# Optimization experiments

Measured on AMD Instinct MI355X. Metric: run time of the kernel, lower is better.

The kernel has to match this reference:

```python
import jax, jax.numpy as jnp
import numpy as np

EPS = 1e-5


def _cbr(z, W, bn, relu=True):
    # z: [b, Cin, L]; W: [Cout, Cin]; bn: [4, Cout] = (gamma, beta, mean, var)
    # 1x1 Conv2d (bias=False) over a [b, Cin, L, 1] tensor == channel matmul.
    y = jnp.einsum('oi,bil->bol', W, z)
    g, b_, m, v = bn[0], bn[1], bn[2], bn[3]
    y = g[:, None] * (y - m[:, None]) * jax.lax.rsqrt(v[:, None] + EPS) + b_[:, None]
    return jax.nn.relu(y) if relu else y


def setup_inputs() -> dict:
    key = jax.random.key(0)
    ks = jax.random.split(key, 13)
    b, c, h, w = 32, 512, 48, 48
    in_spatial = h * w          # 2304
    inter_spatial = in_spatial // 4  # 576
    inter_channel = c // 4      # 128
    ncc = 1 + inter_channel     # 129
    return {
        'x': jax.random.normal(ks[0], (b, c, h, w), jnp.float32),
        'W_theta': jax.random.normal(ks[1], (inter_spatial, in_spatial), jnp.float32) * 0.02,
        'bn_theta': jax.random.uniform(ks[2], (4, inter_spatial), jnp.float32),
        'W_phi': jax.random.normal(ks[3], (inter_spatial, in_spatial), jnp.float32) * 0.02,
        'bn_phi': jax.random.uniform(ks[4], (4, inter_spatial), jnp.float32),
        'W_gx': jax.random.normal(ks[5], (inter_spatial, in_spatial), jnp.float32) * 0.02,
        'bn_gx': jax.random.uniform(ks[6], (4, inter_spatial), jnp.float32),
        'W_gg': jax.random.normal(ks[7], (inter_channel, 2 * c), jnp.float32) * 0.02,
        'bn_gg': jax.random.uniform(ks[8], (4, inter_channel), jnp.float32),
        'W_c1': jax.random.normal(ks[9], (ncc // 2, ncc), jnp.float32) * 0.02,
        'bn_c1': jax.random.uniform(ks[10], (4, ncc // 2), jnp.float32),
        'W_c2': jax.random.normal(ks[11], (1, ncc // 2), jnp.float32) * 0.02,
        'bn_c2': jax.random.uniform(ks[12], (4, 1), jnp.float32),
    }


def reference(x, W_theta, bn_theta, W_phi, bn_phi, W_gx, bn_gx,
              W_gg, bn_gg, W_c1, bn_c1, W_c2, bn_c2):
    b, c, h, w = x.shape
    xc = x.reshape(b, c, h * w).transpose(0, 2, 1)          # [b, hw, c]
    xc1 = _cbr(xc, W_theta, bn_theta).transpose(0, 2, 1)    # [b, c, is]
    xc2 = _cbr(xc, W_phi, bn_phi)                           # [b, is, c]
    Gc = jnp.einsum('bcs,bsd->bcd', xc1, xc2)               # [b, c, c]
    Gc_joint = jnp.concatenate([Gc.transpose(0, 2, 1), Gc], axis=1)  # [b, 2c, c]
    Gc_joint = _cbr(Gc_joint, W_gg, bn_gg)                  # [b, ic, c]
    g_xc = _cbr(xc, W_gx, bn_gx).mean(axis=1, keepdims=True)  # [b, 1, c]
    yc = jnp.concatenate([g_xc, Gc_joint], axis=1)          # [b, 1+ic, c]
    wy = _cbr(yc, W_c1, bn_c1)
    wy = _cbr(wy, W_c2, bn_c2, relu=False)                  # [b, 1, c]
    gate = jax.nn.sigmoid(wy)[:, 0, :, None, None]          # [b, c, 1, 1]
    return gate * x + x
```

## Files before the change

kernel.cpp:

```cpp
#include <hip/hip_runtime.h>
#include <cstdint>

#define EPSV 1e-5f
typedef unsigned short u16;
typedef __attribute__((ext_vector_type(8))) short bh8;
typedef __attribute__((ext_vector_type(4))) float f4;

__device__ __forceinline__ float bf2f(u16 h) { return __uint_as_float((unsigned)h << 16); }
__device__ __forceinline__ u16 f2bf(float x) {
    unsigned u = __float_as_uint(x);
    u += 0x7fffu + ((u >> 16) & 1u);
    return (u16)(u >> 16);
}

__device__ __forceinline__ void gl16(const void* g, const void* s) {
    __builtin_amdgcn_global_load_lds(
        reinterpret_cast<const __attribute__((address_space(1))) void*>((uintptr_t)g),
        reinterpret_cast<__attribute__((address_space(3))) void*>((unsigned)(uintptr_t)s),
        16, 0, 0);
}

__device__ __forceinline__ void core2(
    const u16* __restrict__ Ah, const u16* __restrict__ Al,
    const u16* __restrict__ Bh, const u16* __restrict__ Bl,
    long ldA, long ldB, int K, int rowA0, int rowB0,
    u16* lds, f4 acc[4][4])
{
    const int tid = threadIdx.x, l = tid & 63, w = tid >> 6;
    const int wr = w >> 1, wc = w & 1;
    const int srow = tid >> 2;
    const int schunk = ((tid & 3) ^ ((tid >> 3) & 3)) << 3;
    const size_t aoff = (size_t)(rowA0 + srow) * ldA + schunk;
    const size_t boff = (size_t)(rowB0 + srow) * ldB + schunk;
    const size_t a64 = (size_t)64 * ldA, b64 = (size_t)64 * ldB;
    const int rr = l & 15, cq = l >> 4;
    const int roff = rr * 64 + (((cq ^ ((rr >> 1) & 3))) << 4);
    char* const base0 = (char*)lds;
    char* const base1 = (char*)lds + 32768;
    const int nt = K >> 5;

#define STAGE_SWZ(base, s0) do { \
    gl16(Ah + aoff + (s0),       (base) +         w * 1024); \
    gl16(Ah + aoff + a64 + (s0), (base) +  4096 + w * 1024); \
    gl16(Al + aoff + (s0),       (base) +  8192 + w * 1024); \
    gl16(Al + aoff + a64 + (s0), (base) + 12288 + w * 1024); \
    gl16(Bh + boff + (s0),       (base) + 16384 + w * 1024); \
    gl16(Bh + boff + b64 + (s0), (base) + 20480 + w * 1024); \
    gl16(Bl + boff + (s0),       (base) + 24576 + w * 1024); \
    gl16(Bl + boff + b64 + (s0), (base) + 28672 + w * 1024); \
} while (0)

    STAGE_SWZ(base0, 0);
    __syncthreads();
    int p = 0;
    for (int t = 0; t < nt; ++t) {
        if (t + 1 < nt) STAGE_SWZ(p ? base0 : base1, (size_t)(t + 1) << 5);
        const char* buf = p ? base1 : base0;
        bh8 a_h[4], a_l[4], b_h[4], b_l[4];
#pragma unroll
        for (int i = 0; i < 4; ++i) {
            a_h[i] = *(const bh8*)(buf + (wr * 4 + i) * 1024 + roff);
            a_l[i] = *(const bh8*)(buf + 8192 + (wr * 4 + i) * 1024 + roff);
            b_h[i] = *(const bh8*)(buf + 16384 + (wc * 4 + i) * 1024 + roff);
            b_l[i] = *(const bh8*)(buf + 24576 + (wc * 4 + i) * 1024 + roff);
        }
#pragma unroll
        for (int i = 0; i < 4; ++i)
#pragma unroll
            for (int j = 0; j < 4; ++j)
                acc[i][j] = __builtin_amdgcn_mfma_f32_16x16x32_bf16(a_h[i], b_h[j], acc[i][j], 0, 0, 0);
#pragma unroll
        for (int i = 0; i < 4; ++i)
#pragma unroll
            for (int j = 0; j < 4; ++j)
                acc[i][j] = __builtin_amdgcn_mfma_f32_16x16x32_bf16(a_h[i], b_l[j], acc[i][j], 0, 0, 0);
#pragma unroll
        for (int i = 0; i < 4; ++i)
#pragma unroll
            for (int j = 0; j < 4; ++j)
                acc[i][j] = __builtin_amdgcn_mfma_f32_16x16x32_bf16(a_l[i], b_h[j], acc[i][j], 0, 0, 0);
        __syncthreads();
        p ^= 1;
    }
#undef STAGE_SWZ
}

__device__ __forceinline__ void core3(
    const u16* __restrict__ Ah, const u16* __restrict__ Al,
    const u16* __restrict__ Bh, const u16* __restrict__ Bl,
    long ldA, long ldB, int K, int rowA0, int rowB0, bool full,
    u16* lds, f4 acc[8][4])
{
    const int tid = threadIdx.x, l = tid & 63, w = tid >> 6;
    const int wr = w >> 1, wc = w & 1;
    const int srow = tid >> 2;
    const int schunk = ((tid & 3) ^ ((tid >> 3) & 3)) << 3;
    const size_t aoff = (size_t)(rowA0 + srow) * ldA + schunk;
    const size_t boff = (size_t)(rowB0 + srow) * ldB + schunk;
    const size_t a64 = (size_t)64 * ldA, b64 = (size_t)64 * ldB;
    const int rr = l & 15, cq = l >> 4;
    const int roff = rr * 64 + (((cq ^ ((rr >> 1) & 3))) << 4);
    char* const base0 = (char*)lds;
    char* const base1 = (char*)lds + 49152;
    const int nt = K >> 5;

#define STAGE3(base, s0) do { \
    gl16(Ah + aoff + (s0),           (base) +         w * 1024); \
    gl16(Ah + aoff + a64 + (s0),     (base) +  4096 + w * 1024); \
    gl16(Ah + aoff + 2*a64 + (s0),   (base) +  8192 + w * 1024); \
    gl16(Ah + aoff + 3*a64 + (s0),   (base) + 12288 + w * 1024); \
    if (full) { \
        gl16(Al + aoff + (s0),         (base) + 16384 + w * 1024); \
        gl16(Al + aoff + a64 + (s0),   (base) + 20480 + w * 1024); \
        gl16(Al + aoff + 2*a64 + (s0), (base) + 24576 + w * 1024); \
        gl16(Al + aoff + 3*a64 + (s0), (base) + 28672 + w * 1024); \
    } \
    gl16(Bh + boff + (s0),           (base) + 32768 + w * 1024); \
    gl16(Bh + boff + b64 + (s0),     (base) + 36864 + w * 1024); \
    gl16(Bl + boff + (s0),           (base) + 40960 + w * 1024); \
    gl16(Bl + boff + b64 + (s0),     (base) + 45056 + w * 1024); \
} while (0)

    STAGE3(base0, 0);
    __syncthreads();
    int p = 0;
    for (int t = 0; t < nt; ++t) {
        if (t + 1 < nt) STAGE3(p ? base0 : base1, (size_t)(t + 1) << 5);
        const char* buf = p ? base1 : base0;
        bh8 a_h[8], b_h[4], b_l[4];
#pragma unroll
        for (int i = 0; i < 8; ++i)
            a_h[i] = *(const bh8*)(buf + (wr * 8 + i) * 1024 + roff);
#pragma unroll
        for (int j = 0; j < 4; ++j) {
            b_h[j] = *(const bh8*)(buf + 32768 + (wc * 4 + j) * 1024 + roff);
            b_l[j] = *(const bh8*)(buf + 40960 + (wc * 4 + j) * 1024 + roff);
        }
#pragma unroll
        for (int i = 0; i < 8; ++i)
#pragma unroll
            for (int j = 0; j < 4; ++j)
                acc[i][j] = __builtin_amdgcn_mfma_f32_16x16x32_bf16(a_h[i], b_h[j], acc[i][j], 0, 0, 0);
#pragma unroll
        for (int i = 0; i < 8; ++i)
#pragma unroll
            for (int j = 0; j < 4; ++j)
                acc[i][j] = __builtin_amdgcn_mfma_f32_16x16x32_bf16(a_h[i], b_l[j], acc[i][j], 0, 0, 0);
        if (full) {
            bh8 a_l[8];
#pragma unroll
            for (int i = 0; i < 8; ++i)
                a_l[i] = *(const bh8*)(buf + 16384 + (wr * 8 + i) * 1024 + roff);
#pragma unroll
            for (int i = 0; i < 8; ++i)
#pragma unroll
                for (int j = 0; j < 4; ++j)
                    acc[i][j] = __builtin_amdgcn_mfma_f32_16x16x32_bf16(a_l[i], b_h[j], acc[i][j], 0, 0, 0);
        }
        __syncthreads();
        p ^= 1;
    }
#undef STAGE3
}

__global__ __launch_bounds__(256) void gemm_s1_v4(
    const u16* __restrict__ Xh, const u16* __restrict__ Xl,
    const u16* __restrict__ W0h, const u16* __restrict__ W0l,
    const u16* __restrict__ W1h, const u16* __restrict__ W1l,
    const u16* __restrict__ W2h, const u16* __restrict__ W2l,
    const float* __restrict__ bn0, const float* __restrict__ bn1,
    const float* __restrict__ bn2,
    u16* __restrict__ Y0h, u16* __restrict__ Y0l,
    u16* __restrict__ Y1h, u16* __restrict__ Y1l,
    u16* __restrict__ Y2h, u16* __restrict__ Y2l)
{
    const int h = blockIdx.x;
    const int orig = (h & 7) * 120 + (h >> 3);
    const int ow = orig % 15;
    const int rest = orig / 15;
    const int ct = rest & 1, bz = rest >> 1;
    const int wi = ow / 5, otw = ow % 5;
    const bool full = (wi != 0);

    const u16* Bh = wi == 0 ? W0h : wi == 1 ? W1h : W2h;
    const u16* Bl = wi == 0 ? W0l : wi == 1 ? W1l : W2l;
    const float* bnp = wi == 0 ? bn0 : wi == 1 ? bn1 : bn2;
    u16* Yh = wi == 0 ? Y0h : wi == 1 ? Y1h : Y2h;
    u16* Yl = wi == 0 ? Y0l : wi == 1 ? Y1l : Y2l;

    __shared__ u16 lds[49152];
    f4 acc[8][4];
    const f4 z4 = {0.f, 0.f, 0.f, 0.f};
#pragma unroll
    for (int i = 0; i < 8; ++i)
#pragma unroll
        for (int j = 0; j < 4; ++j) acc[i][j] = z4;

    core3(Xh, Xl, Bh, Bl, 2304, 2304, 2304,
          bz * 512 + ct * 256, otw * 128, full, lds, acc);

    const int l = threadIdx.x & 63, w = threadIdx.x >> 6;
    const int wr = w >> 1, wc = w & 1;
    const int mb = ct * 256 + wr * 128;
    const int nbw = otw * 128 + wc * 64;
    const int lm = l & 15;
#pragma unroll
    for (int j = 0; j < 4; ++j) {
        const int o = nbw + j * 16 + lm;
        const bool val = (o < 576);
        float sc = 0.f, sh = 0.f;
        if (val) {
            const float gg = bnp[o], be = bnp[576 + o], mm = bnp[1152 + o], vv = bnp[1728 + o];
            sc = gg * rsqrtf(vv + EPSV);
            sh = be - mm * sc;
        }
#pragma unroll
        for (int i = 0; i < 8; ++i) {
            const int c = mb + i * 16 + ((l >> 4) << 2);
#pragma unroll
            for (int r = 0; r < 4; ++r) {
                const float y = val ? fmaxf(acc[i][j][r] * sc + sh, 0.f) : 0.f;
                const u16 hh = f2bf(y);
                const u16 lo = f2bf(y - bf2f(hh));
                const size_t off = ((size_t)bz * 512 + c + r) * 640 + o;
                Yh[off] = hh; Yl[off] = lo;
            }
        }
    }
}

__global__ __launch_bounds__(256) void gemm_u(
    const u16* __restrict__ Wggh, const u16* __restrict__ Wggl,
    const u16* __restrict__ tnth, const u16* __restrict__ tntl,
    const u16* __restrict__ pnth, const u16* __restrict__ pntl,
    u16* __restrict__ U1h, u16* __restrict__ U1l,
    u16* __restrict__ U2h, u16* __restrict__ U2l)
{
    const int h = blockIdx.x;
    const int orig = (h & 7) * 40 + (h >> 3);
    const int ot = orig % 5;
    const int rest = orig / 5;
    const int u = rest & 1, b = rest >> 1;

    const u16* Ah = Wggh + (u ? 512 : 0);
    const u16* Al = Wggl + (u ? 512 : 0);
    const u16* Bh = u ? tnth : pnth;
    const u16* Bl = u ? tntl : pntl;

    __shared__ u16 lds[32768];
    f4 acc[4][4];
    const f4 z4 = {0.f, 0.f, 0.f, 0.f};
#pragma unroll
    for (int i = 0; i < 4; ++i)
#pragma unroll
        for (int j = 0; j < 4; ++j) acc[i][j] = z4;

    core2(Ah, Al, Bh, Bl, 1024, 512, 512, 0, b * 640 + ot * 128, lds, acc);

    u16* Uh = u ? U2h : U1h;
    u16* Ul = u ? U2l : U1l;
    const int l = threadIdx.x & 63, w = threadIdx.x >> 6;
    const int wr = w >> 1, wc = w & 1;
#pragma unroll
    for (int i = 0; i < 4; ++i)
#pragma unroll
        for (int j = 0; j < 4; ++j)
#pragma unroll
            for (int r = 0; r < 4; ++r) {
                const int irow = wr * 64 + i * 16 + ((l >> 4) << 2) + r;
                const int ocol = ot * 128 + wc * 64 + j * 16 + (l & 15);
                const float v = acc[i][j][r];
                const u16 hh = f2bf(v);
                const u16 lo = f2bf(v - bf2f(hh));
                const size_t off = ((size_t)b * 128 + irow) * 640 + ocol;
                Uh[off] = hh; Ul[off] = lo;
            }
}

__global__ __launch_bounds__(256) void gemm_term_p(
    const u16* __restrict__ U1h, const u16* __restrict__ U1l,
    const u16* __restrict__ U2h, const u16* __restrict__ U2l,
    const u16* __restrict__ tth, const u16* __restrict__ ttl,
    const u16* __restrict__ pth, const u16* __restrict__ ptl,
    float* __restrict__ GGa, float* __restrict__ GGb)
{
    const int h = blockIdx.x;
    const int orig = (h & 7) * 32 + (h >> 3);
    const int dt = orig & 3;
    const int u = (orig >> 2) & 1;
    const int b = orig >> 3;

    const u16* Ah = u ? U2h : U1h;
    const u16* Al = u ? U2l : U1l;
    const u16* Bh = u ? pth : tth;
    const u16* Bl = u ? ptl : ttl;
    float* G = u ? GGb : GGa;

    __shared__ u16 lds[32768];
    f4 acc[4][4];
    const f4 z4 = {0.f, 0.f, 0.f, 0.f};
#pragma unroll
    for (int i = 0; i < 4; ++i)
#pragma unroll
        for (int j = 0; j < 4; ++j) acc[i][j] = z4;

    core2(Ah, Al, Bh, Bl, 640, 640, 640,
          b * 128, b * 512 + dt * 128, lds, acc);

    const int l = threadIdx.x & 63, w = threadIdx.x >> 6;
    const int wr = w >> 1, wc = w & 1;
#pragma unroll
    for (int i = 0; i < 4; ++i)
#pragma unroll
        for (int j = 0; j < 4; ++j)
#pragma unroll
            for (int r = 0; r < 4; ++r) {
                const int irow = wr * 64 + i * 16 + ((l >> 4) << 2) + r;
                const int dcol = dt * 128 + wc * 64 + j * 16 + (l & 15);
                G[((size_t)b * 128 + irow) * 512 + dcol] = acc[i][j][r];
            }
}

__global__ __launch_bounds__(256) void gg_combine(
    float* __restrict__ GGa, const float* __restrict__ GGb,
    const float* __restrict__ bn, long n4)
{
    const long i = (long)blockIdx.x * 256 + threadIdx.x;
    if (i >= n4) return;
    const int irow = (int)((i >> 7) & 127);
    const float g = bn[irow], be = bn[128 + irow], m = bn[256 + irow], v = bn[384 + irow];
    const float sc = g * rsqrtf(v + EPSV);
    const float sh = be - m * sc;
    float4 a = ((const float4*)GGa)[i];
    const float4 b = ((const float4*)GGb)[i];
    a.x = fmaxf((a.x + b.x) * sc + sh, 0.f);
    a.y = fmaxf((a.y + b.y) * sc + sh, 0.f);
    a.z = fmaxf((a.z + b.z) * sc + sh, 0.f);
    a.w = fmaxf((a.w + b.w) * sc + sh, 0.f);
    ((float4*)GGa)[i] = a;
}

__global__ __launch_bounds__(256) void transpose_y(
    const u16* __restrict__ s0, u16* __restrict__ d0,
    const u16* __restrict__ s1, u16* __restrict__ d1,
    const u16* __restrict__ s2, u16* __restrict__ d2,
    const u16* __restrict__ s3, u16* __restrict__ d3)
{
    const int pz = blockIdx.z;
    const int b = pz >> 2, pl = pz & 3;
    const u16* src = pl == 0 ? s0 : pl == 1 ? s1 : pl == 2 ? s2 : s3;
    u16* dst = pl == 0 ? d0 : pl == 1 ? d1 : pl == 2 ? d2 : d3;
    const int o0 = blockIdx.x * 64, c0 = blockIdx.y * 64;
    __shared__ u16 t[64][72];
    const int tid = threadIdx.x;
#pragma unroll
    for (int rdx = tid; rdx < 512; rdx += 256) {
        const int c = rdx >> 3, oc = (rdx & 7) << 3;
        *(bh8*)&t[c][oc] = *(const bh8*)&src[((size_t)b * 512 + c0 + c) * 640 + o0 + oc];
    }
    __syncthreads();
#pragma unroll
    for (int wdx = tid; wdx < 512; wdx += 256) {
        const int o = wdx >> 3, cc = (wdx & 7) << 3;
        u16 v[8];
#pragma unroll
        for (int e = 0; e < 8; ++e) v[e] = t[cc + e][o];
        *(bh8*)&dst[((size_t)b * 640 + o0 + o) * 512 + c0 + cc] = *(bh8*)&v[0];
    }
}

__global__ __launch_bounds__(256) void conv_split(
    const float* __restrict__ in, u16* __restrict__ hi, u16* __restrict__ lo, long n8)
{
    long i = (long)blockIdx.x * 256 + threadIdx.x;
    const long stride = (long)gridDim.x * 256;
    for (; i < n8; i += stride) {
        const float4 a = ((const float4*)in)[2 * i];
        const float4 b = ((const float4*)in)[2 * i + 1];
        const float v[8] = {a.x, a.y, a.z, a.w, b.x, b.y, b.z, b.w};
        unsigned hw[4], lw[4];
#pragma unroll
        for (int k = 0; k < 4; ++k) {
            const u16 h0 = f2bf(v[2 * k]), h1 = f2bf(v[2 * k + 1]);
            const u16 l0 = f2bf(v[2 * k] - bf2f(h0)), l1 = f2bf(v[2 * k + 1] - bf2f(h1));
            hw[k] = (unsigned)h0 | ((unsigned)h1 << 16);
            lw[k] = (unsigned)l0 | ((unsigned)l1 << 16);
        }
        *(uint4*)&hi[8 * i] = make_uint4(hw[0], hw[1], hw[2], hw[3]);
        *(uint4*)&lo[8 * i] = make_uint4(lw[0], lw[1], lw[2], lw[3]);
    }
}

__global__ __launch_bounds__(256) void conv_w_pad(
    const float* __restrict__ W, u16* __restrict__ hi, u16* __restrict__ lo,
    int rows, long n8)
{
    const long i = (long)blockIdx.x * 256 + threadIdx.x;
    if (i >= n8) return;
    const long e = i * 8;
    const int row = (int)(e / 2304);
    unsigned hw[4] = {0, 0, 0, 0}, lw[4] = {0, 0, 0, 0};
    if (row < rows) {
        const float4 a = ((const float4*)W)[2 * i];
        const float4 b = ((const float4*)W)[2 * i + 1];
        const float v[8] = {a.x, a.y, a.z, a.w, b.x, b.y, b.z, b.w};
#pragma unroll
        for (int k = 0; k < 4; ++k) {
            const u16 h0 = f2bf(v[2 * k]), h1 = f2bf(v[2 * k + 1]);
            const u16 l0 = f2bf(v[2 * k] - bf2f(h0)), l1 = f2bf(v[2 * k + 1] - bf2f(h1));
            hw[k] = (unsigned)h0 | ((unsigned)h1 << 16);
            lw[k] = (unsigned)l0 | ((unsigned)l1 << 16);
        }
    }
    *(uint4*)&hi[8 * i] = make_uint4(hw[0], hw[1], hw[2], hw[3]);
    *(uint4*)&lo[8 * i] = make_uint4(lw[0], lw[1], lw[2], lw[3]);
}

__global__ __launch_bounds__(256) void row_mean(
    const u16* __restrict__ Yh, const u16* __restrict__ Yl,
    float* __restrict__ out, int rows)
{
    const int l = threadIdx.x & 63;
    const int row = blockIdx.x * 4 + (threadIdx.x >> 6);
    if (row >= rows) return;
    const u16* ph = Yh + (size_t)row * 640;
    const u16* pl = Yl + (size_t)row * 640;
    float s = 0.f;
    struct U8 { u16 u[8]; };
    for (int k = l; k < 80; k += 64) {
        const U8 a = *(const U8*)&ph[k * 8];
        const U8 b = *(const U8*)&pl[k * 8];
#pragma unroll
        for (int e = 0; e < 8; ++e) s += bf2f(a.u[e]) + bf2f(b.u[e]);
    }
    for (int off = 32; off; off >>= 1) s += __shfl_down(s, off, 64);
    if (l == 0) out[row] = s * (1.f / 576.f);
}

__global__ __launch_bounds__(256)
void gate_kernel(const float* __restrict__ gxc, const float* __restrict__ GG,
                 const float* __restrict__ Wc1, const float* __restrict__ bn1,
                 const float* __restrict__ Wc2, const float* __restrict__ bn2,
                 float* __restrict__ gate, int IC, int D, int OC)
{
    const int b  = blockIdx.y;
    const int d0 = blockIdx.x * 64;

    __shared__ float yc_s[129][64];
    __shared__ float part[4][64];

    const int tid = threadIdx.x;
    for (int idx = tid; idx < 129 * 64; idx += 256) {
        const int j = idx >> 6, d = idx & 63;
        yc_s[j][d] = (j == 0) ? gxc[b * D + d0 + d]
                              : GG[((size_t)b * IC + (j - 1)) * D + d0 + d];
    }
    __syncthreads();

    const int d = tid & 63;
    const int q = tid >> 6;
    float acc2 = 0.f;
    for (int o = q * 16; o < q * 16 + 16; ++o) {
        float s = 0.f;
        const float* __restrict__ w = &Wc1[o * 129];
        for (int j = 0; j < 129; ++j) s = fmaf(w[j], yc_s[j][d], s);
        const float g1 = bn1[o], be1 = bn1[OC + o], m1 = bn1[2 * OC + o], v1 = bn1[3 * OC + o];
        const float sc = g1 / sqrtf(v1 + EPSV);
        const float w1 = fmaxf(s * sc + (be1 - m1 * sc), 0.f);
        acc2 = fmaf(Wc2[o], w1, acc2);
    }
    part[q][d] = acc2;
    __syncthreads();
    if (q == 0) {
        const float s = part[0][d] + part[1][d] + part[2][d] + part[3][d];
        const float g2 = bn2[0], be2 = bn2[1], m2 = bn2[2], v2 = bn2[3];
        const float sc = g2 / sqrtf(v2 + EPSV);
        const float wy = s * sc + (be2 - m2 * sc);
        gate[b * D + d0 + d] = 1.f / (1.f + expf(-wy));
    }
}

__global__ __launch_bounds__(256)
void final_kernel(const float* __restrict__ x, const float* __restrict__ gate,
                  float* __restrict__ out, long n4, int sp4)
{
    long i = (long)blockIdx.x * blockDim.x + threadIdx.x;
    const long stride = (long)gridDim.x * blockDim.x;
    for (; i < n4; i += stride) {
        float4 v = ((const float4*)x)[i];
        const long bc = i / sp4;
        const float gm = 1.f + gate[bc];
        v.x *= gm; v.y *= gm; v.z *= gm; v.w *= gm;
        ((float4*)out)[i] = v;
    }
}

extern "C" void kernel_launch(void* const* d_in, const int* in_sizes, int n_in,
                              void* d_out, int out_size, void* d_ws, size_t ws_size,
                              hipStream_t stream)
{
    const float* x        = (const float*)d_in[0];
    const float* W_theta  = (const float*)d_in[1];
    const float* bn_theta = (const float*)d_in[2];
    const float* W_phi    = (const float*)d_in[3];
    const float* bn_phi   = (const float*)d_in[4];
    const float* W_gx     = (const float*)d_in[5];
    const float* bn_gx    = (const float*)d_in[6];
    const float* W_gg     = (const float*)d_in[7];
    const float* bn_gg    = (const float*)d_in[8];
    const float* W_c1     = (const float*)d_in[9];
    const float* bn_c1    = (const float*)d_in[10];
    const float* W_c2     = (const float*)d_in[11];
    const float* bn_c2    = (const float*)d_in[12];
    float* out = (float*)d_out;

    const int B = 32, C = 512, S = 2304, O = 576, OP = 640, IC = 128, OC = 64;
    const size_t P  = (size_t)B * C * OP;
    const size_t WP = (size_t)OP * S;
    const size_t UP = (size_t)B * IC * OP;

    u16* tth = (u16*)d_out;
    u16* ttl = tth + P;
    u16* pth = ttl + P;
    u16* ptl = pth + P;
    u16* Wgh = ptl + P;
    u16* Wgl = Wgh + WP;
    u16* Wth = Wgl + WP;
    u16* Wtl = Wth + WP;
    u16* Wph = Wtl + WP;
    u16* Wpl = Wph + WP;
    u16* wggh = Wpl + WP;
    u16* wggl = wggh + (size_t)IC * 1024;
    u16* u1h = wggl + (size_t)IC * 1024;
    u16* u1l = u1h + UP;
    u16* u2h = u1l + UP;
    u16* u2l = u2h + UP;
    float* GGa = (float*)(u2l + UP);
    float* GGb = GGa + (size_t)B * IC * C;

    u16* Xhi  = (u16*)d_ws;
    u16* Xlo  = Xhi + (size_t)B * C * S;
    u16* ygxh = Xlo + (size_t)B * C * S;
    u16* ygxl = ygxh + P;
    float* gxc  = (float*)(ygxl + P);
    float* gate = gxc + (size_t)B * C;
    u16* tnth = (u16*)d_ws;
    u16* tntl = tnth + P;
    u16* pnth = tntl + P;
    u16* pntl = pnth + P;

    const dim3 blk(256);

    const long wN8 = (long)WP / 8;
    conv_w_pad<<<dim3((unsigned)(wN8 / 256)), blk, 0, stream>>>(W_gx,    Wgh, Wgl, O, wN8);
    conv_w_pad<<<dim3((unsigned)(wN8 / 256)), blk, 0, stream>>>(W_theta, Wth, Wtl, O, wN8);
    conv_w_pad<<<dim3((unsigned)(wN8 / 256)), blk, 0, stream>>>(W_phi,   Wph, Wpl, O, wN8);
    conv_split<<<dim3(64), blk, 0, stream>>>(W_gg, wggh, wggl, (long)IC * 1024 / 8);

    conv_split<<<dim3(2048), blk, 0, stream>>>(x, Xhi, Xlo, (long)B * C * S / 8);
    gemm_s1_v4<<<dim3(960), blk, 0, stream>>>(
        Xhi, Xlo, Wgh, Wgl, Wth, Wtl, Wph, Wpl,
        bn_gx, bn_theta, bn_phi,
        ygxh, ygxl, tth, ttl, pth, ptl);
    row_mean<<<dim3(4096), blk, 0, stream>>>(ygxh, ygxl, gxc, B * C);

    transpose_y<<<dim3(10, 8, 128), blk, 0, stream>>>(
        tth, tnth, ttl, tntl, pth, pnth, ptl, pntl);

    gemm_u<<<dim3(320), blk, 0, stream>>>(wggh, wggl, tnth, tntl, pnth, pntl,
                                          u1h, u1l, u2h, u2l);

    gemm_term_p<<<dim3(256), blk, 0, stream>>>(u1h, u1l, u2h, u2l,
                                               tth, ttl, pth, ptl, GGa, GGb);
    gg_combine<<<dim3(2048), blk, 0, stream>>>(GGa, GGb, bn_gg,
                                               (long)B * IC * C / 4);

    gate_kernel<<<dim3(C / 64, B), blk, 0, stream>>>(gxc, GGa, W_c1, bn_c1, W_c2, bn_c2,
                                                     gate, IC, C, OC);

    final_kernel<<<dim3(2048), blk, 0, stream>>>(x, gate, out,
                                                 (long)B * C * S / 4, S / 4);
}
```

Measured before the change: 680.6 us.

## Single-buffer LDS in stage-1 GEMM with mid-iteration prefetch to raise occupancy

The stage-1 GEMM core drops the double-buffered LDS (96KB) in favour of a single 48KB buffer. All fragments, including the low A parts, are read into registers first. After the first MFMA group a barrier is taken and the next tile's global-to-LDS load is issued, overlapping with the remaining MFMAs. This halves LDS use so more workgroups can share a CU, at the cost of an extra barrier per iteration, less load/compute overlap, and higher register pressure from holding a_l early.

```diff
diff --git a/kernel.cpp b/kernel.cpp
--- a/kernel.cpp
+++ b/kernel.cpp
@@ -85,7 +85,7 @@
 #undef STAGE_SWZ
 }
 
-__device__ __forceinline__ void core3(
+__device__ __forceinline__ void core3r(
     const u16* __restrict__ Ah, const u16* __restrict__ Al,
     const u16* __restrict__ Bh, const u16* __restrict__ Bl,
     long ldA, long ldB, int K, int rowA0, int rowB0, bool full,
@@ -100,57 +100,56 @@
     const size_t a64 = (size_t)64 * ldA, b64 = (size_t)64 * ldB;
     const int rr = l & 15, cq = l >> 4;
     const int roff = rr * 64 + (((cq ^ ((rr >> 1) & 3))) << 4);
-    char* const base0 = (char*)lds;
-    char* const base1 = (char*)lds + 49152;
+    char* const base = (char*)lds;
     const int nt = K >> 5;
 
-#define STAGE3(base, s0) do { \
-    gl16(Ah + aoff + (s0),           (base) +         w * 1024); \
-    gl16(Ah + aoff + a64 + (s0),     (base) +  4096 + w * 1024); \
-    gl16(Ah + aoff + 2*a64 + (s0),   (base) +  8192 + w * 1024); \
-    gl16(Ah + aoff + 3*a64 + (s0),   (base) + 12288 + w * 1024); \
+#define STAGE3(s0) do { \
+    gl16(Ah + aoff + (s0),           base +         w * 1024); \
+    gl16(Ah + aoff + a64 + (s0),     base +  4096 + w * 1024); \
+    gl16(Ah + aoff + 2*a64 + (s0),   base +  8192 + w * 1024); \
+    gl16(Ah + aoff + 3*a64 + (s0),   base + 12288 + w * 1024); \
     if (full) { \
-        gl16(Al + aoff + (s0),         (base) + 16384 + w * 1024); \
-        gl16(Al + aoff + a64 + (s0),   (base) + 20480 + w * 1024); \
-        gl16(Al + aoff + 2*a64 + (s0), (base) + 24576 + w * 1024); \
-        gl16(Al + aoff + 3*a64 + (s0), (base) + 28672 + w * 1024); \
+        gl16(Al + aoff + (s0),         base + 16384 + w * 1024); \
+        gl16(Al + aoff + a64 + (s0),   base + 20480 + w * 1024); \
+        gl16(Al + aoff + 2*a64 + (s0), base + 24576 + w * 1024); \
+        gl16(Al + aoff + 3*a64 + (s0), base + 28672 + w * 1024); \
     } \
-    gl16(Bh + boff + (s0),           (base) + 32768 + w * 1024); \
-    gl16(Bh + boff + b64 + (s0),     (base) + 36864 + w * 1024); \
-    gl16(Bl + boff + (s0),           (base) + 40960 + w * 1024); \
-    gl16(Bl + boff + b64 + (s0),     (base) + 45056 + w * 1024); \
+    gl16(Bh + boff + (s0),           base + 32768 + w * 1024); \
+    gl16(Bh + boff + b64 + (s0),     base + 36864 + w * 1024); \
+    gl16(Bl + boff + (s0),           base + 40960 + w * 1024); \
+    gl16(Bl + boff + b64 + (s0),     base + 45056 + w * 1024); \
 } while (0)
 
-    STAGE3(base0, 0);
+    STAGE3(0);
     __syncthreads();
-    int p = 0;
     for (int t = 0; t < nt; ++t) {
-        if (t + 1 < nt) STAGE3(p ? base0 : base1, (size_t)(t + 1) << 5);
-        const char* buf = p ? base1 : base0;
-        bh8 a_h[8], b_h[4], b_l[4];
+        bh8 a_h[8], a_l[8], b_h[4], b_l[4];
 #pragma unroll
         for (int i = 0; i < 8; ++i)
-            a_h[i] = *(const bh8*)(buf + (wr * 8 + i) * 1024 + roff);
+            a_h[i] = *(const bh8*)(base + (wr * 8 + i) * 1024 + roff);
+        if (full) {
+#pragma unroll
+            for (int i = 0; i < 8; ++i)
+                a_l[i] = *(const bh8*)(base + 16384 + (wr * 8 + i) * 1024 + roff);
+        }
 #pragma unroll
         for (int j = 0; j < 4; ++j) {
-            b_h[j] = *(const bh8*)(buf + 32768 + (wc * 4 + j) * 1024 + roff);
-            b_l[j] = *(const bh8*)(buf + 40960 + (wc * 4 + j) * 1024 + roff);
+            b_h[j] = *(const bh8*)(base + 32768 + (wc * 4 + j) * 1024 + roff);
+            b_l[j] = *(const bh8*)(base + 40960 + (wc * 4 + j) * 1024 + roff);
         }
 #pragma unroll
         for (int i = 0; i < 8; ++i)
 #pragma unroll
             for (int j = 0; j < 4; ++j)
                 acc[i][j] = __builtin_amdgcn_mfma_f32_16x16x32_bf16(a_h[i], b_h[j], acc[i][j], 0, 0, 0);
+        __syncthreads();
+        if (t + 1 < nt) STAGE3((size_t)(t + 1) << 5);
 #pragma unroll
         for (int i = 0; i < 8; ++i)
 #pragma unroll
             for (int j = 0; j < 4; ++j)
                 acc[i][j] = __builtin_amdgcn_mfma_f32_16x16x32_bf16(a_h[i], b_l[j], acc[i][j], 0, 0, 0);
         if (full) {
-            bh8 a_l[8];
-#pragma unroll
-            for (int i = 0; i < 8; ++i)
-                a_l[i] = *(const bh8*)(buf + 16384 + (wr * 8 + i) * 1024 + roff);
 #pragma unroll
             for (int i = 0; i < 8; ++i)
 #pragma unroll
@@ -158,12 +157,11 @@
                     acc[i][j] = __builtin_amdgcn_mfma_f32_16x16x32_bf16(a_l[i], b_h[j], acc[i][j], 0, 0, 0);
         }
         __syncthreads();
-        p ^= 1;
     }
 #undef STAGE3
 }
 
-__global__ __launch_bounds__(256) void gemm_s1_v4(
+__global__ __launch_bounds__(256) void gemm_s1_v5(
     const u16* __restrict__ Xh, const u16* __restrict__ Xl,
     const u16* __restrict__ W0h, const u16* __restrict__ W0l,
     const u16* __restrict__ W1h, const u16* __restrict__ W1l,
@@ -188,7 +186,7 @@
     u16* Yh = wi == 0 ? Y0h : wi == 1 ? Y1h : Y2h;
     u16* Yl = wi == 0 ? Y0l : wi == 1 ? Y1l : Y2l;
 
-    __shared__ u16 lds[49152];
+    __shared__ u16 lds[24576];
     f4 acc[8][4];
     const f4 z4 = {0.f, 0.f, 0.f, 0.f};
 #pragma unroll
@@ -196,8 +194,8 @@
 #pragma unroll
         for (int j = 0; j < 4; ++j) acc[i][j] = z4;
 
-    core3(Xh, Xl, Bh, Bl, 2304, 2304, 2304,
-          bz * 512 + ct * 256, otw * 128, full, lds, acc);
+    core3r(Xh, Xl, Bh, Bl, 2304, 2304, 2304,
+           bz * 512 + ct * 256, otw * 128, full, lds, acc);
 
     const int l = threadIdx.x & 63, w = threadIdx.x >> 6;
     const int wr = w >> 1, wc = w & 1;
@@ -558,7 +556,7 @@
     conv_split<<<dim3(64), blk, 0, stream>>>(W_gg, wggh, wggl, (long)IC * 1024 / 8);
 
     conv_split<<<dim3(2048), blk, 0, stream>>>(x, Xhi, Xlo, (long)B * C * S / 8);
-    gemm_s1_v4<<<dim3(960), blk, 0, stream>>>(
+    gemm_s1_v5<<<dim3(960), blk, 0, stream>>>(
         Xhi, Xlo, Wgh, Wgl, Wth, Wtl, Wph, Wpl,
         bn_gx, bn_theta, bn_phi,
         ygxh, ygxl, tth, ttl, pth, ptl);
```

Measured after the change: 663.9 us. -2.5%, faster.
